# Kernel tuning notes

Measured on AMD Instinct MI355X. Metric: run time of the kernel, lower is better.

Reference implementation:

```python
import jax, jax.numpy as jnp
import numpy as np

N, E, IN_DIM, HID, HEADS = 50000, 800000, 128, 16, 8
EPS_BN = 1e-5


def _gat_conv(x, edge_index, W, att_src, att_dst, bias, heads, out_ch, concat):
    # x: [N, F_in]; W: [heads*out_ch, F_in]; att_*: [heads, out_ch]
    n = x.shape[0]
    h = (x @ W.T).reshape(n, heads, out_ch)            # [N, H, C]
    a_src = (h * att_src[None]).sum(-1)                # [N, H]
    a_dst = (h * att_dst[None]).sum(-1)                # [N, H]
    src, dst = edge_index[0], edge_index[1]
    alpha = jax.nn.leaky_relu(a_src[src] + a_dst[dst], negative_slope=0.2)  # [E, H]
    # segment softmax over destination node (per head)
    amax = jax.ops.segment_max(alpha, dst, num_segments=n)
    amax = jnp.where(jnp.isfinite(amax), amax, 0.0)
    ex = jnp.exp(alpha - amax[dst])
    denom = jax.ops.segment_sum(ex, dst, num_segments=n)
    attn = ex / (denom[dst] + 1e-16)                   # [E, H]
    msg = h[src] * attn[:, :, None]                    # [E, H, C]
    out = jax.ops.segment_sum(msg, dst, num_segments=n)  # [N, H, C]
    out = out.reshape(n, heads * out_ch) if concat else out.mean(axis=1)
    return out + bias


def _bn_eval(h, mean, var, gamma, beta):
    return (h - mean) * jax.lax.rsqrt(var + EPS_BN) * gamma + beta


def setup_inputs() -> dict:
    key = jax.random.key(0)
    ks = jax.random.split(key, 16)
    s = 0.1
    inp = {
        "x": jax.random.normal(ks[0], (N, IN_DIM), jnp.float32),
        "edge_index": jax.random.randint(ks[1], (2, E), 0, N, jnp.int32),
        # layer 0: GATConv(128 -> 16, heads=8, concat)
        "w0": jax.random.normal(ks[2], (HEADS * HID, IN_DIM), jnp.float32) * s,
        "asrc0": jax.random.normal(ks[3], (HEADS, HID), jnp.float32) * s,
        "adst0": jax.random.normal(ks[4], (HEADS, HID), jnp.float32) * s,
        "b0": jnp.zeros((HEADS * HID,), jnp.float32),
        "skip0": jax.random.normal(ks[5], (HEADS * HID, IN_DIM), jnp.float32) * s,
        "bn0_g": jnp.ones((HEADS * HID,), jnp.float32),
        "bn0_b": jnp.zeros((HEADS * HID,), jnp.float32),
        "bn0_m": jax.random.normal(ks[6], (HEADS * HID,), jnp.float32) * s,
        "bn0_v": jax.random.uniform(ks[7], (HEADS * HID,), jnp.float32, 0.5, 1.5),
        # layer 1: GATConv(128 -> 16, heads=1, concat=False)
        "w1": jax.random.normal(ks[8], (HID, HEADS * HID), jnp.float32) * s,
        "asrc1": jax.random.normal(ks[9], (1, HID), jnp.float32) * s,
        "adst1": jax.random.normal(ks[10], (1, HID), jnp.float32) * s,
        "b1": jnp.zeros((HID,), jnp.float32),
        "skip1": jax.random.normal(ks[11], (HID, HEADS * HID), jnp.float32) * s,
        "bn1_g": jnp.ones((HID,), jnp.float32),
        "bn1_b": jnp.zeros((HID,), jnp.float32),
        "bn1_m": jax.random.normal(ks[12], (HID,), jnp.float32) * s,
        "bn1_v": jax.random.uniform(ks[13], (HID,), jnp.float32, 0.5, 1.5),
    }
    return inp


def reference(x, edge_index, w0, asrc0, adst0, b0, skip0, bn0_g, bn0_b, bn0_m, bn0_v,
              w1, asrc1, adst1, b1, skip1, bn1_g, bn1_b, bn1_m, bn1_v):
    # eval mode: dropout = identity, BN uses running stats
    h_in = x
    h = _gat_conv(h_in, edge_index, w0, asrc0, adst0, b0, HEADS, HID, True)   # [N, 128]
    h = _bn_eval(h, bn0_m, bn0_v, bn0_g, bn0_b)
    h = h + h_in @ skip0.T
    h = jax.nn.elu(h)
    h_in = h
    h = _gat_conv(h_in, edge_index, w1, asrc1, adst1, b1, 1, HID, False)      # [N, 16]
    h = _bn_eval(h, bn1_m, bn1_v, bn1_g, bn1_b)
    h = h + h_in @ skip1.T
    h = jax.nn.elu(h)
    return h
```

## Files before the change

### kernel.cpp

```cpp
#include <hip/hip_runtime.h>
#include <hip/hip_bf16.h>

#define NN 50000
#define EE 800000
#define INDIM 128
#define HIDC 16
#define NHEAD 8
#define COARSE 196
#define EPB 2048
#define CAPR 6144
#define CAPB 8192

typedef __attribute__((ext_vector_type(8))) short bf16x8;
typedef __attribute__((ext_vector_type(4))) float f32x4;

__device__ __forceinline__ float bf2f(unsigned short u) {
    union { float f; unsigned int i; } v; v.i = ((unsigned int)u) << 16; return v.f;
}
__device__ __forceinline__ unsigned short f2bf(float f) {
    union { float f; unsigned int i; } v; v.f = f;
    unsigned int r = v.i + 0x7FFFu + ((v.i >> 16) & 1u);
    return (unsigned short)(r >> 16);
}

__global__ __launch_bounds__(256) void k_cvt(const float* __restrict__ x,
                                             const float* __restrict__ w0,
                                             const float* __restrict__ skip0,
                                             const float* __restrict__ w1,
                                             const float* __restrict__ skip1,
                                             unsigned int* __restrict__ xb2,
                                             unsigned int* __restrict__ wb2,
                                             unsigned int* __restrict__ wb1_2,
                                             int* __restrict__ ccur)
{
    if (blockIdx.x == 0 && threadIdx.x < COARSE)
        ccur[threadIdx.x] = threadIdx.x * CAPR;

    const long NX = (long)NN * 128 / 4;
    const long NW = 256 * 128 / 4;
    const long NW1 = 32 * 128 / 4;
    long i = (long)blockIdx.x * 256 + threadIdx.x;
    if (i < NX) {
        float4 v = ((const float4*)x)[i];
        xb2[i * 2]     = (unsigned int)f2bf(v.x) | ((unsigned int)f2bf(v.y) << 16);
        xb2[i * 2 + 1] = (unsigned int)f2bf(v.z) | ((unsigned int)f2bf(v.w) << 16);
    } else if (i < NX + NW) {
        long j = i - NX;
        const float4* src = (j < 128 * 128 / 4) ? ((const float4*)w0 + j)
                                                : ((const float4*)skip0 + (j - 128 * 128 / 4));
        float4 v = *src;
        wb2[j * 2]     = (unsigned int)f2bf(v.x) | ((unsigned int)f2bf(v.y) << 16);
        wb2[j * 2 + 1] = (unsigned int)f2bf(v.z) | ((unsigned int)f2bf(v.w) << 16);
    } else if (i < NX + NW + NW1) {
        long j = i - NX - NW;
        const float4* src = (j < 16 * 128 / 4) ? ((const float4*)w1 + j)
                                               : ((const float4*)skip1 + (j - 16 * 128 / 4));
        float4 v = *src;
        wb1_2[j * 2]     = (unsigned int)f2bf(v.x) | ((unsigned int)f2bf(v.y) << 16);
        wb1_2[j * 2 + 1] = (unsigned int)f2bf(v.z) | ((unsigned int)f2bf(v.w) << 16);
    }
}

__global__ __launch_bounds__(256) void k_partA(const int* __restrict__ ei,
                                               int* __restrict__ ccur,
                                               unsigned int* __restrict__ pairs)
{
    __shared__ int bcnt[256];
    __shared__ int lofs[256];
    __shared__ int gofs[256];
    __shared__ unsigned int stage[EPB];
    __shared__ int gpos[EPB];
    const int t = threadIdx.x;
    const int e0 = blockIdx.x * EPB;

    bcnt[t] = 0;
    __syncthreads();

    int mybin[8], myrank[8];
    unsigned int mypair[8];
    #pragma unroll
    for (int k = 0; k < 8; k++) {
        int e = e0 + k * 256 + t;
        mybin[k] = -1;
        if (e < EE) {
            int s = ei[e], d = ei[EE + e];
            int b = d >> 8;
            myrank[k] = atomicAdd(&bcnt[b], 1);
            mybin[k] = b;
            mypair[k] = ((unsigned)d << 16) | (unsigned)s;
        }
    }
    __syncthreads();

    int v = bcnt[t];
    lofs[t] = v;
    __syncthreads();
    for (int off = 1; off < 256; off <<= 1) {
        int u = (t >= off) ? lofs[t - off] : 0;
        __syncthreads();
        lofs[t] += u;
        __syncthreads();
    }
    if (t < COARSE && v > 0) gofs[t] = atomicAdd(&ccur[t], v);
    __syncthreads();

    #pragma unroll
    for (int k = 0; k < 8; k++) {
        int b = mybin[k];
        if (b >= 0) {
            int slot = (lofs[b] - bcnt[b]) + myrank[k];
            stage[slot] = mypair[k];
            gpos[slot]  = gofs[b] + myrank[k];
        }
    }
    __syncthreads();

    const int total = lofs[255];
    for (int i = t; i < total; i += 256)
        pairs[gpos[i]] = stage[i];
}

__global__ __launch_bounds__(256) void k_partB(const unsigned int* __restrict__ pairs,
                                               const int* __restrict__ ccur,
                                               unsigned short* __restrict__ srcidx,
                                               int* __restrict__ rowbeg,
                                               int* __restrict__ deg)
{
    __shared__ int fcnt[256], fofs[256], fcur[256];
    __shared__ unsigned short stage[CAPB];
    const int b = blockIdx.x, t = threadIdx.x;
    const int beg = b * CAPR;
    int cnt = ccur[b] - beg;
    if (cnt > CAPR) cnt = CAPR;

    fcnt[t] = 0;
    __syncthreads();
    for (int i = t; i < cnt; i += 256) {
        unsigned int d = pairs[beg + i] >> 16;
        atomicAdd(&fcnt[d & 255], 1);
    }
    __syncthreads();

    int v = fcnt[t];
    fofs[t] = v;
    __syncthreads();
    for (int off = 1; off < 256; off <<= 1) {
        int u = (t >= off) ? fofs[t - off] : 0;
        __syncthreads();
        fofs[t] += u;
        __syncthreads();
    }
    int ex = fofs[t] - v;
    int node = b * 256 + t;
    if (node < NN) { rowbeg[node] = beg + ex; deg[node] = v; }
    fcur[t] = ex;
    __syncthreads();

    for (int i = t; i < cnt; i += 256) {
        unsigned int p = pairs[beg + i];
        unsigned int d = p >> 16;
        int slot = atomicAdd(&fcur[d & 255], 1);
        stage[slot] = (unsigned short)(p & 0xFFFFu);
    }
    __syncthreads();
    for (int i = t; i < cnt; i += 256)
        srcidx[beg + i] = stage[i];
}

__global__ __launch_bounds__(256) void k_gemm0(
    const unsigned short* __restrict__ xb, const unsigned short* __restrict__ wb,
    const float* __restrict__ asrc0, const float* __restrict__ adst0,
    unsigned char* __restrict__ h0f, unsigned short* __restrict__ s0b,
    float* __restrict__ a_src0, float* __restrict__ a_dst0)
{
    const int wave = threadIdx.x >> 6;
    const int lane = threadIdx.x & 63;
    const int lrow = lane & 15;
    const int quad = lane >> 4;
    const int rowbase = blockIdx.x * 32;

    bf16x8 bfrag[4][4];
    float4 asv[4], adv[4];
    #pragma unroll
    for (int t = 0; t < 4; t++) {
        const int jg = wave * 64 + t * 16 + lrow;
        #pragma unroll
        for (int ki = 0; ki < 4; ki++)
            bfrag[t][ki] = *(const bf16x8*)(wb + (long)jg * 128 + ki * 32 + quad * 8);
        if (wave < 2) {
            const int cb = wave * 64 + t * 16 + quad * 4;
            asv[t] = *(const float4*)(asrc0 + cb);
            adv[t] = *(const float4*)(adst0 + cb);
        }
    }

    #pragma unroll
    for (int sub = 0; sub < 2; sub++) {
        const int row0 = rowbase + sub * 16;
        if (row0 >= NN) break;
        const unsigned short* xrow = xb + (long)(row0 + lrow) * 128;
        bf16x8 afrag[4];
        #pragma unroll
        for (int ki = 0; ki < 4; ki++)
            afrag[ki] = *(const bf16x8*)(xrow + ki * 32 + quad * 8);

        f32x4 acc[4];
        #pragma unroll
        for (int t = 0; t < 4; t++) acc[t] = (f32x4){0.f, 0.f, 0.f, 0.f};

        #pragma unroll
        for (int ki = 0; ki < 4; ki++)
            #pragma unroll
            for (int t = 0; t < 4; t++)
                acc[t] = __builtin_amdgcn_mfma_f32_16x16x32_bf16(bfrag[t][ki], afrag[ki], acc[t], 0, 0, 0);

        const int node = row0 + lrow;
        if (wave < 2) {
            #pragma unroll
            for (int t = 0; t < 4; t++) {
                const int cb = wave * 64 + t * 16 + quad * 4;
                unsigned int u = __builtin_amdgcn_cvt_pk_fp8_f32(acc[t][0], acc[t][1], 0u, 0);
                u = __builtin_amdgcn_cvt_pk_fp8_f32(acc[t][2], acc[t][3], u, 1);
                *(unsigned int*)(h0f + (long)node * 128 + cb) = u;
                float ps = acc[t][0] * asv[t].x + acc[t][1] * asv[t].y
                         + acc[t][2] * asv[t].z + acc[t][3] * asv[t].w;
                float pd = acc[t][0] * adv[t].x + acc[t][1] * adv[t].y
                         + acc[t][2] * adv[t].z + acc[t][3] * adv[t].w;
                ps += __shfl_xor(ps, 16); ps += __shfl_xor(ps, 32);
                pd += __shfl_xor(pd, 16); pd += __shfl_xor(pd, 32);
                if (quad == 0) {
                    const int h = wave * 4 + t;
                    a_src0[(long)node * 8 + h] = ps;
                    a_dst0[(long)node * 8 + h] = pd;
                }
            }
        } else {
            #pragma unroll
            for (int t = 0; t < 4; t++) {
                const int cb = (wave - 2) * 64 + t * 16 + quad * 4;
                uint2 u;
                u.x = (unsigned int)f2bf(acc[t][0]) | ((unsigned int)f2bf(acc[t][1]) << 16);
                u.y = (unsigned int)f2bf(acc[t][2]) | ((unsigned int)f2bf(acc[t][3]) << 16);
                *(uint2*)(s0b + (long)node * 128 + cb) = u;
            }
        }
    }
}

__global__ __launch_bounds__(256) void k_agg0(
    const int* __restrict__ rowbeg, const int* __restrict__ deg,
    const unsigned short* __restrict__ srcidx,
    const unsigned char* __restrict__ h0f, const float* __restrict__ a_src0,
    const float* __restrict__ a_dst0, unsigned int* __restrict__ out0b2)
{
    const int d = (blockIdx.x * 256 + threadIdx.x) >> 6;
    if (d >= NN) return;
    const int lane = threadIdx.x & 63;
    const int beg = rowbeg[d], end = beg + deg[d];
    const int eslot = lane >> 3;
    const int hph1 = lane & 7;
    const int c = lane * 2;
    const int hsel = lane >> 3;
    const float adst = a_dst0[(long)d * 8 + hph1];

    float den = 0.f;
    float2 accA = {0.f, 0.f}, accB = {0.f, 0.f};
    for (int i = beg; i < end; i += 16) {
        const int idxA = i + eslot;
        const int idxB = i + 8 + eslot;
        const bool vA = idxA < end;
        const bool vB = idxB < end;
        const int sA = vA ? (int)srcidx[idxA] : 0;
        const int sB = vB ? (int)srcidx[idxB] : 0;
        float aA = a_src0[(long)sA * 8 + hph1] + adst;
        float aB = a_src0[(long)sB * 8 + hph1] + adst;
        aA = aA > 0.f ? aA : 0.2f * aA;
        aB = aB > 0.f ? aB : 0.2f * aB;
        const float wA = vA ? __expf(aA) : 0.f;
        const float wB = vB ? __expf(aB) : 0.f;
        den += wA + wB;
        #pragma unroll
        for (int j = 0; j < 8; j++) {
            const float wjA = __shfl(wA, j * 8 + hsel);
            const int sjA = __shfl(sA, j * 8);
            const float wjB = __shfl(wB, j * 8 + hsel);
            const int sjB = __shfl(sB, j * 8);
            const unsigned int uA = *(const unsigned short*)(h0f + (long)sjA * 128 + c);
            const unsigned int uB = *(const unsigned short*)(h0f + (long)sjB * 128 + c);
            accA.x += wjA * __builtin_amdgcn_cvt_f32_fp8(uA, 0);
            accA.y += wjA * __builtin_amdgcn_cvt_f32_fp8(uA, 1);
            accB.x += wjB * __builtin_amdgcn_cvt_f32_fp8(uB, 0);
            accB.y += wjB * __builtin_amdgcn_cvt_f32_fp8(uB, 1);
        }
    }
    float2 acc = {accA.x + accB.x, accA.y + accB.y};
    den += __shfl_xor(den, 8);
    den += __shfl_xor(den, 16);
    den += __shfl_xor(den, 32);
    const float denh = __shfl(den, hsel);
    const float inv = 1.f / (denh + 1e-16f);
    out0b2[(long)d * 64 + lane] =
        (unsigned int)f2bf(acc.x * inv) | ((unsigned int)f2bf(acc.y * inv) << 16);
}

__global__ __launch_bounds__(256) void k_post0(
    const unsigned short* __restrict__ out0b, const unsigned short* __restrict__ s0b,
    const float* __restrict__ b0, const float* __restrict__ g0,
    const float* __restrict__ bb0, const float* __restrict__ m0,
    const float* __restrict__ v0,
    const unsigned short* __restrict__ wb1,
    const float* __restrict__ asrc1, const float* __restrict__ adst1,
    unsigned short* __restrict__ h1b, float* __restrict__ s1,
    float* __restrict__ a_src1, float* __restrict__ a_dst1)
{
    __shared__ float Ac[128], Bc[128];
    const int tid = threadIdx.x;
    if (tid < 128) {
        float A = g0[tid] * rsqrtf(v0[tid] + 1e-5f);
        Ac[tid] = A;
        Bc[tid] = (b0[tid] - m0[tid]) * A + bb0[tid];
    }
    __syncthreads();

    const int lane = tid & 63, wave = tid >> 6;
    const int lrow = lane & 15, quad = lane >> 4;

    bf16x8 bfrag[2][4];
    #pragma unroll
    for (int t = 0; t < 2; t++)
        #pragma unroll
        for (int ki = 0; ki < 4; ki++)
            bfrag[t][ki] = *(const bf16x8*)(wb1 + (long)(t * 16 + lrow) * 128 + ki * 32 + quad * 8);
    const float avec = asrc1[lrow];
    const float dvec = adst1[lrow];

    const int tile = blockIdx.x * 4 + wave;
    if (tile * 16 >= NN) return;
    const int n0 = tile * 16;
    const long arow = (long)(n0 + lrow) * 128;

    bf16x8 afrag[4];
    #pragma unroll
    for (int ki = 0; ki < 4; ki++) {
        const int ch = ki * 32 + quad * 8;
        uint4 uo = *(const uint4*)(out0b + arow + ch);
        uint4 us = *(const uint4*)(s0b + arow + ch);
        const unsigned int uov[4] = {uo.x, uo.y, uo.z, uo.w};
        const unsigned int usv[4] = {us.x, us.y, us.z, us.w};
        bf16x8 af;
        #pragma unroll
        for (int e = 0; e < 4; e++) {
            const int c0 = ch + e * 2, c1 = c0 + 1;
            float x0 = bf2f((unsigned short)uov[e]) * Ac[c0] + Bc[c0] + bf2f((unsigned short)usv[e]);
            float x1 = bf2f((unsigned short)(uov[e] >> 16)) * Ac[c1] + Bc[c1] + bf2f((unsigned short)(usv[e] >> 16));
            x0 = x0 > 0.f ? x0 : __expf(x0) - 1.f;
            x1 = x1 > 0.f ? x1 : __expf(x1) - 1.f;
            af[e * 2]     = (short)f2bf(x0);
            af[e * 2 + 1] = (short)f2bf(x1);
        }
        afrag[ki] = af;
    }

    f32x4 acc0 = (f32x4){0.f, 0.f, 0.f, 0.f};
    f32x4 acc1 = (f32x4){0.f, 0.f, 0.f, 0.f};
    #pragma unroll
    for (int ki = 0; ki < 4; ki++) {
        acc0 = __builtin_amdgcn_mfma_f32_16x16x32_bf16(afrag[ki], bfrag[0][ki], acc0, 0, 0, 0);
        acc1 = __builtin_amdgcn_mfma_f32_16x16x32_bf16(afrag[ki], bfrag[1][ki], acc1, 0, 0, 0);
    }

    #pragma unroll
    for (int r = 0; r < 4; r++) {
        const int node = n0 + quad * 4 + r;
        h1b[(long)node * 16 + lrow] = f2bf(acc0[r]);
        s1[(long)node * 16 + lrow] = acc1[r];
        float ps = acc0[r] * avec;
        float pd = acc0[r] * dvec;
        ps += __shfl_xor(ps, 1); ps += __shfl_xor(ps, 2);
        ps += __shfl_xor(ps, 4); ps += __shfl_xor(ps, 8);
        pd += __shfl_xor(pd, 1); pd += __shfl_xor(pd, 2);
        pd += __shfl_xor(pd, 4); pd += __shfl_xor(pd, 8);
        if (lrow == 0) { a_src1[node] = ps; a_dst1[node] = pd; }
    }
}

__global__ __launch_bounds__(256) void k_agg1_final(
    const int* __restrict__ rowbeg, const int* __restrict__ deg,
    const unsigned short* __restrict__ srcidx,
    const unsigned short* __restrict__ h1b, const float* __restrict__ a_src1,
    const float* __restrict__ a_dst1, const float* __restrict__ s1,
    const float* __restrict__ b1, const float* __restrict__ g1,
    const float* __restrict__ bb1, const float* __restrict__ m1,
    const float* __restrict__ v1, float* __restrict__ out)
{
    const int gid = blockIdx.x * 256 + threadIdx.x;
    const int d = gid >> 3;
    if (d >= NN) return;
    const int lane = threadIdx.x & 63;
    const int gl = lane & 7;
    const int gb = lane & ~7;
    const int c0 = gl * 2, c1 = c0 + 1;
    const int beg = rowbeg[d], end = beg + deg[d];
    const float adst = a_dst1[d];

    float den = 0.f;
    float2 accA = {0.f, 0.f}, accB = {0.f, 0.f};
    for (int i = beg; i < end; i += 16) {
        const int idxA = i + gl;
        const int idxB = i + 8 + gl;
        const bool vA = idxA < end;
        const bool vB = idxB < end;
        const int sA = vA ? (int)srcidx[idxA] : 0;
        const int sB = vB ? (int)srcidx[idxB] : 0;
        float aA = a_src1[sA] + adst;
        float aB = a_src1[sB] + adst;
        aA = aA > 0.f ? aA : 0.2f * aA;
        aB = aB > 0.f ? aB : 0.2f * aB;
        const float wA = vA ? __expf(aA) : 0.f;
        const float wB = vB ? __expf(aB) : 0.f;
        den += wA + wB;
        #pragma unroll
        for (int j = 0; j < 8; j++) {
            const float wjA = __shfl(wA, gb | j);
            const int sjA = __shfl(sA, gb | j);
            const float wjB = __shfl(wB, gb | j);
            const int sjB = __shfl(sB, gb | j);
            const unsigned int uA = *(const unsigned int*)(h1b + (long)sjA * 16 + c0);
            const unsigned int uB = *(const unsigned int*)(h1b + (long)sjB * 16 + c0);
            accA.x += wjA * bf2f((unsigned short)uA);
            accA.y += wjA * bf2f((unsigned short)(uA >> 16));
            accB.x += wjB * bf2f((unsigned short)uB);
            accB.y += wjB * bf2f((unsigned short)(uB >> 16));
        }
    }
    float2 acc = {accA.x + accB.x, accA.y + accB.y};
    den += __shfl_xor(den, 1);
    den += __shfl_xor(den, 2);
    den += __shfl_xor(den, 4);
    const float inv = 1.f / (den + 1e-16f);

    const float A0 = g1[c0] * rsqrtf(v1[c0] + 1e-5f);
    const float B0 = (b1[c0] - m1[c0]) * A0 + bb1[c0];
    const float A1 = g1[c1] * rsqrtf(v1[c1] + 1e-5f);
    const float B1 = (b1[c1] - m1[c1]) * A1 + bb1[c1];
    float2 sv = *(const float2*)(s1 + (long)d * 16 + c0);
    float v0o = acc.x * inv * A0 + B0 + sv.x;
    float v1o = acc.y * inv * A1 + B1 + sv.y;
    v0o = v0o > 0.f ? v0o : __expf(v0o) - 1.f;
    v1o = v1o > 0.f ? v1o : __expf(v1o) - 1.f;
    *(float2*)(out + (long)d * 16 + c0) = make_float2(v0o, v1o);
}

extern "C" void kernel_launch(void* const* d_in, const int* in_sizes, int n_in,
                              void* d_out, int out_size, void* d_ws, size_t ws_size,
                              hipStream_t stream)
{
    (void)in_sizes; (void)n_in; (void)out_size; (void)ws_size;
    const float* x     = (const float*)d_in[0];
    const int*   ei    = (const int*)d_in[1];
    const float* w0    = (const float*)d_in[2];
    const float* asrc0 = (const float*)d_in[3];
    const float* adst0 = (const float*)d_in[4];
    const float* b0    = (const float*)d_in[5];
    const float* skip0 = (const float*)d_in[6];
    const float* bn0g  = (const float*)d_in[7];
    const float* bn0b  = (const float*)d_in[8];
    const float* bn0m  = (const float*)d_in[9];
    const float* bn0v  = (const float*)d_in[10];
    const float* w1    = (const float*)d_in[11];
    const float* asrc1 = (const float*)d_in[12];
    const float* adst1 = (const float*)d_in[13];
    const float* b1    = (const float*)d_in[14];
    const float* skip1 = (const float*)d_in[15];
    const float* bn1g  = (const float*)d_in[16];
    const float* bn1b  = (const float*)d_in[17];
    const float* bn1m  = (const float*)d_in[18];
    const float* bn1v  = (const float*)d_in[19];

    const long NPAIR = (long)COARSE * CAPR;
    unsigned int* pairs = (unsigned int*)d_ws;
    unsigned short* xb    = (unsigned short*)(pairs + NPAIR);
    unsigned short* wb    = xb + (long)NN * 128;
    unsigned short* wb1   = wb + 256 * 128;
    unsigned short* s0b   = wb1 + 32 * 128;
    unsigned short* out0b = s0b + (long)NN * 128;
    unsigned short* h1b   = out0b + (long)NN * 128;
    unsigned short* srcidx= h1b + (long)NN * 16;
    unsigned char*  h0f   = (unsigned char*)(srcidx + NPAIR);
    float* a_src0 = (float*)(h0f + (long)NN * 128);
    float* a_dst0 = a_src0 + (long)NN * 8;
    float* s1     = a_dst0 + (long)NN * 8;
    float* a_src1 = s1 + (long)NN * 16;
    float* a_dst1 = a_src1 + NN;
    int* ccur   = (int*)(a_dst1 + NN);
    int* rowbeg = ccur + COARSE;
    int* deg    = rowbeg + NN;

    const long NTOT = (long)NN * 128 / 4 + 256 * 128 / 4 + 32 * 128 / 4;
    k_cvt<<<(unsigned)((NTOT + 255) / 256), 256, 0, stream>>>(
        x, w0, skip0, w1, skip1,
        (unsigned int*)xb, (unsigned int*)wb, (unsigned int*)wb1, ccur);

    k_partA<<<(EE + EPB - 1) / EPB, 256, 0, stream>>>(ei, ccur, pairs);
    k_partB<<<COARSE, 256, 0, stream>>>(pairs, ccur, srcidx, rowbeg, deg);

    k_gemm0<<<(NN + 31) / 32, 256, 0, stream>>>(xb, wb, asrc0, adst0,
                                                h0f, s0b, a_src0, a_dst0);
    k_agg0<<<(NN * 64 + 255) / 256, 256, 0, stream>>>(rowbeg, deg, srcidx, h0f,
                                                      a_src0, a_dst0, (unsigned int*)out0b);
    k_post0<<<(NN / 16 + 3) / 4, 256, 0, stream>>>(out0b, s0b, b0, bn0g, bn0b, bn0m, bn0v,
                                                   wb1, asrc1, adst1, h1b, s1, a_src1, a_dst1);
    k_agg1_final<<<(NN * 8 + 255) / 256, 256, 0, stream>>>(rowbeg, deg, srcidx, h1b,
                                                           a_src1, a_dst1, s1,
                                                           b1, bn1g, bn1b, bn1m, bn1v,
                                                           (float*)d_out);
}
```

Baseline: 218.5 us.

## Fuse BN, skip-add and ELU into layer-0 aggregation and restructure gemm0 loops

Precomputes the folded batch-norm scale/shift for both layers once in the conversion kernel instead of per block or per thread. The layer-0 BN, skip-connection add and ELU move into the aggregation kernel, so the post kernel just loads ready bf16 activations and no longer reads the separate skip tensor. The layer-0 GEMM is reordered to hold both row tiles of A in registers and stream weight fragments per output tile, which lowers register pressure. In exchange the aggregation kernel does more work per node and reads s0b.

Result: no change. 216.3 us (-1.0%).

```diff
diff --git a/kernel.cpp b/kernel.cpp
--- a/kernel.cpp
+++ b/kernel.cpp
@@ -28,9 +28,21 @@
                                              const float* __restrict__ skip0,
                                              const float* __restrict__ w1,
                                              const float* __restrict__ skip1,
+                                             const float* __restrict__ b0,
+                                             const float* __restrict__ g0,
+                                             const float* __restrict__ bb0,
+                                             const float* __restrict__ m0,
+                                             const float* __restrict__ v0,
+                                             const float* __restrict__ b1,
+                                             const float* __restrict__ g1,
+                                             const float* __restrict__ bb1,
+                                             const float* __restrict__ m1,
+                                             const float* __restrict__ v1,
                                              unsigned int* __restrict__ xb2,
                                              unsigned int* __restrict__ wb2,
                                              unsigned int* __restrict__ wb1_2,
+                                             float2* __restrict__ acb0,
+                                             float2* __restrict__ acb1,
                                              int* __restrict__ ccur)
 {
     if (blockIdx.x == 0 && threadIdx.x < COARSE)
@@ -58,6 +70,14 @@
         float4 v = *src;
         wb1_2[j * 2]     = (unsigned int)f2bf(v.x) | ((unsigned int)f2bf(v.y) << 16);
         wb1_2[j * 2 + 1] = (unsigned int)f2bf(v.z) | ((unsigned int)f2bf(v.w) << 16);
+    } else if (i < NX + NW + NW1 + 128) {
+        int c = (int)(i - NX - NW - NW1);
+        float A = g0[c] * rsqrtf(v0[c] + 1e-5f);
+        acb0[c] = make_float2(A, (b0[c] - m0[c]) * A + bb0[c]);
+    } else if (i < NX + NW + NW1 + 128 + 16) {
+        int c = (int)(i - NX - NW - NW1 - 128);
+        float A = g1[c] * rsqrtf(v1[c] + 1e-5f);
+        acb1[c] = make_float2(A, (b1[c] - m1[c]) * A + bb1[c]);
     }
 }
 
@@ -179,69 +199,59 @@
     const int quad = lane >> 4;
     const int rowbase = blockIdx.x * 32;
 
-    bf16x8 bfrag[4][4];
-    float4 asv[4], adv[4];
+    bf16x8 afrag[2][4];
+    #pragma unroll
+    for (int sub = 0; sub < 2; sub++) {
+        const int row = min(rowbase + sub * 16 + lrow, NN - 1);
+        const unsigned short* xrow = xb + (long)row * 128;
+        #pragma unroll
+        for (int ki = 0; ki < 4; ki++)
+            afrag[sub][ki] = *(const bf16x8*)(xrow + ki * 32 + quad * 8);
+    }
+
     #pragma unroll
     for (int t = 0; t < 4; t++) {
         const int jg = wave * 64 + t * 16 + lrow;
+        bf16x8 bfrag[4];
         #pragma unroll
         for (int ki = 0; ki < 4; ki++)
-            bfrag[t][ki] = *(const bf16x8*)(wb + (long)jg * 128 + ki * 32 + quad * 8);
+            bfrag[ki] = *(const bf16x8*)(wb + (long)jg * 128 + ki * 32 + quad * 8);
+        float4 asv = {0.f, 0.f, 0.f, 0.f}, adv = {0.f, 0.f, 0.f, 0.f};
         if (wave < 2) {
             const int cb = wave * 64 + t * 16 + quad * 4;
-            asv[t] = *(const float4*)(asrc0 + cb);
-            adv[t] = *(const float4*)(adst0 + cb);
+            asv = *(const float4*)(asrc0 + cb);
+            adv = *(const float4*)(adst0 + cb);
         }
-    }
-
-    #pragma unroll
-    for (int sub = 0; sub < 2; sub++) {
-        const int row0 = rowbase + sub * 16;
-        if (row0 >= NN) break;
-        const unsigned short* xrow = xb + (long)(row0 + lrow) * 128;
-        bf16x8 afrag[4];
         #pragma unroll
-        for (int ki = 0; ki < 4; ki++)
-            afrag[ki] = *(const bf16x8*)(xrow + ki * 32 + quad * 8);
-
-        f32x4 acc[4];
-        #pragma unroll
-        for (int t = 0; t < 4; t++) acc[t] = (f32x4){0.f, 0.f, 0.f, 0.f};
-
-        #pragma unroll
-        for (int ki = 0; ki < 4; ki++)
+        for (int sub = 0; sub < 2; sub++) {
+            f32x4 acc = (f32x4){0.f, 0.f, 0.f, 0.f};
             #pragma unroll
-            for (int t = 0; t < 4; t++)
-                acc[t] = __builtin_amdgcn_mfma_f32_16x16x32_bf16(bfrag[t][ki], afrag[ki], acc[t], 0, 0, 0);
-
-        const int node = row0 + lrow;
-        if (wave < 2) {
-            #pragma unroll
-            for (int t = 0; t < 4; t++) {
-                const int cb = wave * 64 + t * 16 + quad * 4;
-                unsigned int u = __builtin_amdgcn_cvt_pk_fp8_f32(acc[t][0], acc[t][1], 0u, 0);
-                u = __builtin_amdgcn_cvt_pk_fp8_f32(acc[t][2], acc[t][3], u, 1);
-                *(unsigned int*)(h0f + (long)node * 128 + cb) = u;
-                float ps = acc[t][0] * asv[t].x + acc[t][1] * asv[t].y
-                         + acc[t][2] * asv[t].z + acc[t][3] * asv[t].w;
-                float pd = acc[t][0] * adv[t].x + acc[t][1] * adv[t].y
-                         + acc[t][2] * adv[t].z + acc[t][3] * adv[t].w;
-                ps += __shfl_xor(ps, 16); ps += __shfl_xor(ps, 32);
-                pd += __shfl_xor(pd, 16); pd += __shfl_xor(pd, 32);
-                if (quad == 0) {
-                    const int h = wave * 4 + t;
-                    a_src0[(long)node * 8 + h] = ps;
-                    a_dst0[(long)node * 8 + h] = pd;
+            for (int ki = 0; ki < 4; ki++)
+                acc = __builtin_amdgcn_mfma_f32_16x16x32_bf16(bfrag[ki], afrag[sub][ki], acc, 0, 0, 0);
+
+            const int node = rowbase + sub * 16 + lrow;
+            if (node < NN) {
+                if (wave < 2) {
+                    const int cb = wave * 64 + t * 16 + quad * 4;
+                    unsigned int u = __builtin_amdgcn_cvt_pk_fp8_f32(acc[0], acc[1], 0u, 0);
+                    u = __builtin_amdgcn_cvt_pk_fp8_f32(acc[2], acc[3], u, 1);
+                    *(unsigned int*)(h0f + (long)node * 128 + cb) = u;
+                    float ps = acc[0] * asv.x + acc[1] * asv.y + acc[2] * asv.z + acc[3] * asv.w;
+                    float pd = acc[0] * adv.x + acc[1] * adv.y + acc[2] * adv.z + acc[3] * adv.w;
+                    ps += __shfl_xor(ps, 16); ps += __shfl_xor(ps, 32);
+                    pd += __shfl_xor(pd, 16); pd += __shfl_xor(pd, 32);
+                    if (quad == 0) {
+                        const int h = wave * 4 + t;
+                        a_src0[(long)node * 8 + h] = ps;
+                        a_dst0[(long)node * 8 + h] = pd;
+                    }
+                } else {
+                    const int cb = (wave - 2) * 64 + t * 16 + quad * 4;
+                    uint2 u;
+                    u.x = (unsigned int)f2bf(acc[0]) | ((unsigned int)f2bf(acc[1]) << 16);
+                    u.y = (unsigned int)f2bf(acc[2]) | ((unsigned int)f2bf(acc[3]) << 16);
+                    *(uint2*)(s0b + (long)node * 128 + cb) = u;
                 }
-            }
-        } else {
-            #pragma unroll
-            for (int t = 0; t < 4; t++) {
-                const int cb = (wave - 2) * 64 + t * 16 + quad * 4;
-                uint2 u;
-                u.x = (unsigned int)f2bf(acc[t][0]) | ((unsigned int)f2bf(acc[t][1]) << 16);
-                u.y = (unsigned int)f2bf(acc[t][2]) | ((unsigned int)f2bf(acc[t][3]) << 16);
-                *(uint2*)(s0b + (long)node * 128 + cb) = u;
             }
         }
     }
@@ -251,7 +261,8 @@
     const int* __restrict__ rowbeg, const int* __restrict__ deg,
     const unsigned short* __restrict__ srcidx,
     const unsigned char* __restrict__ h0f, const float* __restrict__ a_src0,
-    const float* __restrict__ a_dst0, unsigned int* __restrict__ out0b2)
+    const float* __restrict__ a_dst0, const unsigned short* __restrict__ s0b,
+    const float2* __restrict__ acb0, unsigned int* __restrict__ hab2)
 {
     const int d = (blockIdx.x * 256 + threadIdx.x) >> 6;
     if (d >= NN) return;
@@ -299,29 +310,25 @@
     den += __shfl_xor(den, 32);
     const float denh = __shfl(den, hsel);
     const float inv = 1.f / (denh + 1e-16f);
-    out0b2[(long)d * 64 + lane] =
-        (unsigned int)f2bf(acc.x * inv) | ((unsigned int)f2bf(acc.y * inv) << 16);
+
+    const float4 ab = *(const float4*)((const float*)acb0 + 2 * c);
+    const unsigned int s0u = *(const unsigned int*)(s0b + (long)d * 128 + c);
+    float x0 = acc.x * inv * ab.x + ab.y + bf2f((unsigned short)s0u);
+    float x1 = acc.y * inv * ab.z + ab.w + bf2f((unsigned short)(s0u >> 16));
+    x0 = x0 > 0.f ? x0 : __expf(x0) - 1.f;
+    x1 = x1 > 0.f ? x1 : __expf(x1) - 1.f;
+    hab2[(long)d * 64 + lane] =
+        (unsigned int)f2bf(x0) | ((unsigned int)f2bf(x1) << 16);
 }
 
 __global__ __launch_bounds__(256) void k_post0(
-    const unsigned short* __restrict__ out0b, const unsigned short* __restrict__ s0b,
-    const float* __restrict__ b0, const float* __restrict__ g0,
-    const float* __restrict__ bb0, const float* __restrict__ m0,
-    const float* __restrict__ v0,
+    const unsigned short* __restrict__ hab,
     const unsigned short* __restrict__ wb1,
     const float* __restrict__ asrc1, const float* __restrict__ adst1,
     unsigned short* __restrict__ h1b, float* __restrict__ s1,
     float* __restrict__ a_src1, float* __restrict__ a_dst1)
 {
-    __shared__ float Ac[128], Bc[128];
     const int tid = threadIdx.x;
-    if (tid < 128) {
-        float A = g0[tid] * rsqrtf(v0[tid] + 1e-5f);
-        Ac[tid] = A;
-        Bc[tid] = (b0[tid] - m0[tid]) * A + bb0[tid];
-    }
-    __syncthreads();
-
     const int lane = tid & 63, wave = tid >> 6;
     const int lrow = lane & 15, quad = lane >> 4;
 
@@ -341,25 +348,8 @@
 
     bf16x8 afrag[4];
     #pragma unroll
-    for (int ki = 0; ki < 4; ki++) {
-        const int ch = ki * 32 + quad * 8;
-        uint4 uo = *(const uint4*)(out0b + arow + ch);
-        uint4 us = *(const uint4*)(s0b + arow + ch);
-        const unsigned int uov[4] = {uo.x, uo.y, uo.z, uo.w};
-        const unsigned int usv[4] = {us.x, us.y, us.z, us.w};
-        bf16x8 af;
-        #pragma unroll
-        for (int e = 0; e < 4; e++) {
-            const int c0 = ch + e * 2, c1 = c0 + 1;
-            float x0 = bf2f((unsigned short)uov[e]) * Ac[c0] + Bc[c0] + bf2f((unsigned short)usv[e]);
-            float x1 = bf2f((unsigned short)(uov[e] >> 16)) * Ac[c1] + Bc[c1] + bf2f((unsigned short)(usv[e] >> 16));
-            x0 = x0 > 0.f ? x0 : __expf(x0) - 1.f;
-            x1 = x1 > 0.f ? x1 : __expf(x1) - 1.f;
-            af[e * 2]     = (short)f2bf(x0);
-            af[e * 2 + 1] = (short)f2bf(x1);
-        }
-        afrag[ki] = af;
-    }
+    for (int ki = 0; ki < 4; ki++)
+        afrag[ki] = *(const bf16x8*)(hab + arow + ki * 32 + quad * 8);
 
     f32x4 acc0 = (f32x4){0.f, 0.f, 0.f, 0.f};
     f32x4 acc1 = (f32x4){0.f, 0.f, 0.f, 0.f};
@@ -389,9 +379,7 @@
     const unsigned short* __restrict__ srcidx,
     const unsigned short* __restrict__ h1b, const float* __restrict__ a_src1,
     const float* __restrict__ a_dst1, const float* __restrict__ s1,
-    const float* __restrict__ b1, const float* __restrict__ g1,
-    const float* __restrict__ bb1, const float* __restrict__ m1,
-    const float* __restrict__ v1, float* __restrict__ out)
+    const float2* __restrict__ acb1, float* __restrict__ out)
 {
     const int gid = blockIdx.x * 256 + threadIdx.x;
     const int d = gid >> 3;
@@ -399,7 +387,7 @@
     const int lane = threadIdx.x & 63;
     const int gl = lane & 7;
     const int gb = lane & ~7;
-    const int c0 = gl * 2, c1 = c0 + 1;
+    const int c0 = gl * 2;
     const int beg = rowbeg[d], end = beg + deg[d];
     const float adst = a_dst1[d];
 
@@ -439,13 +427,10 @@
     den += __shfl_xor(den, 4);
     const float inv = 1.f / (den + 1e-16f);
 
-    const float A0 = g1[c0] * rsqrtf(v1[c0] + 1e-5f);
-    const float B0 = (b1[c0] - m1[c0]) * A0 + bb1[c0];
-    const float A1 = g1[c1] * rsqrtf(v1[c1] + 1e-5f);
-    const float B1 = (b1[c1] - m1[c1]) * A1 + bb1[c1];
+    const float4 ab = *(const float4*)((const float*)acb1 + 2 * c0);
     float2 sv = *(const float2*)(s1 + (long)d * 16 + c0);
-    float v0o = acc.x * inv * A0 + B0 + sv.x;
-    float v1o = acc.y * inv * A1 + B1 + sv.y;
+    float v0o = acc.x * inv * ab.x + ab.y + sv.x;
+    float v1o = acc.y * inv * ab.z + ab.w + sv.y;
     v0o = v0o > 0.f ? v0o : __expf(v0o) - 1.f;
     v1o = v1o > 0.f ? v1o : __expf(v1o) - 1.f;
     *(float2*)(out + (long)d * 16 + c0) = make_float2(v0o, v1o);
@@ -483,8 +468,8 @@
     unsigned short* wb    = xb + (long)NN * 128;
     unsigned short* wb1   = wb + 256 * 128;
     unsigned short* s0b   = wb1 + 32 * 128;
-    unsigned short* out0b = s0b + (long)NN * 128;
-    unsigned short* h1b   = out0b + (long)NN * 128;
+    unsigned short* hab   = s0b + (long)NN * 128;
+    unsigned short* h1b   = hab + (long)NN * 128;
     unsigned short* srcidx= h1b + (long)NN * 16;
     unsigned char*  h0f   = (unsigned char*)(srcidx + NPAIR);
     float* a_src0 = (float*)(h0f + (long)NN * 128);
@@ -492,14 +477,18 @@
     float* s1     = a_dst0 + (long)NN * 8;
     float* a_src1 = s1 + (long)NN * 16;
     float* a_dst1 = a_src1 + NN;
-    int* ccur   = (int*)(a_dst1 + NN);
+    float2* acb0  = (float2*)(a_dst1 + NN);
+    float2* acb1  = acb0 + 128;
+    int* ccur   = (int*)(acb1 + 16);
     int* rowbeg = ccur + COARSE;
     int* deg    = rowbeg + NN;
 
-    const long NTOT = (long)NN * 128 / 4 + 256 * 128 / 4 + 32 * 128 / 4;
+    const long NTOT = (long)NN * 128 / 4 + 256 * 128 / 4 + 32 * 128 / 4 + 144;
     k_cvt<<<(unsigned)((NTOT + 255) / 256), 256, 0, stream>>>(
         x, w0, skip0, w1, skip1,
-        (unsigned int*)xb, (unsigned int*)wb, (unsigned int*)wb1, ccur);
+        b0, bn0g, bn0b, bn0m, bn0v, b1, bn1g, bn1b, bn1m, bn1v,
+        (unsigned int*)xb, (unsigned int*)wb, (unsigned int*)wb1,
+        acb0, acb1, ccur);
 
     k_partA<<<(EE + EPB - 1) / EPB, 256, 0, stream>>>(ei, ccur, pairs);
     k_partB<<<COARSE, 256, 0, stream>>>(pairs, ccur, srcidx, rowbeg, deg);
@@ -507,11 +496,11 @@
     k_gemm0<<<(NN + 31) / 32, 256, 0, stream>>>(xb, wb, asrc0, adst0,
                                                 h0f, s0b, a_src0, a_dst0);
     k_agg0<<<(NN * 64 + 255) / 256, 256, 0, stream>>>(rowbeg, deg, srcidx, h0f,
-                                                      a_src0, a_dst0, (unsigned int*)out0b);
-    k_post0<<<(NN / 16 + 3) / 4, 256, 0, stream>>>(out0b, s0b, b0, bn0g, bn0b, bn0m, bn0v,
-                                                   wb1, asrc1, adst1, h1b, s1, a_src1, a_dst1);
+                                                      a_src0, a_dst0, s0b, acb0,
+                                                      (unsigned int*)hab);
+    k_post0<<<(NN / 16 + 3) / 4, 256, 0, stream>>>(hab, wb1, asrc1, adst1,
+                                                   h1b, s1, a_src1, a_dst1);
     k_agg1_final<<<(NN * 8 + 255) / 256, 256, 0, stream>>>(rowbeg, deg, srcidx, h1b,
                                                            a_src1, a_dst1, s1,
-                                                           b1, bn1g, bn1b, bn1m, bn1v,
-                                                           (float*)d_out);
-}
+                                                           acb1, (float*)d_out);
+}
```
